# Performance work log

Measured on AMD Instinct MI355X. Metric: run time of the kernel, lower is better.

## Reference

```python
import jax, jax.numpy as jnp
import numpy as np

B, S, H, NH = 4, 2048, 768, 12
PH = H // NH  # per-head size


def setup_inputs() -> dict:
    key = jax.random.key(0)
    ks = jax.random.split(key, 12)
    s = 0.02
    return {
        "key": jax.random.normal(ks[0], (B, S, H), jnp.float32),
        "value": jax.random.normal(ks[1], (B, S, H), jnp.float32),
        "query": jax.random.normal(ks[2], (B, S, H), jnp.float32),
        "mask": jnp.zeros((B, 1, S, S), jnp.float32),  # additive mask
        "Wq": jax.random.normal(ks[3], (H, H), jnp.float32) * s,
        "bq": jnp.zeros((H,), jnp.float32),
        "Wk": jax.random.normal(ks[4], (H, H), jnp.float32) * s,
        "bk": jnp.zeros((H,), jnp.float32),
        "Wv": jax.random.normal(ks[5], (H, H), jnp.float32) * s,
        "bv": jnp.zeros((H,), jnp.float32),
        "Wo": jax.random.normal(ks[6], (H, H), jnp.float32) * s,
        "bo": jnp.zeros((H,), jnp.float32),
    }


def _heads(x):
    # [B,S,H] -> [B,NH,S,PH]
    return x.reshape(B, S, NH, PH).transpose(0, 2, 1, 3)


def reference(key, value, query, mask, Wq, bq, Wk, bk, Wv, bv, Wo, bo):
    # torch Linear: y = x @ W.T + b  (separate projections for q, k, v)
    q = _heads(query @ Wq.T + bq)
    k = _heads(key @ Wk.T + bk)
    v = _heads(value @ Wv.T + bv)
    scale = 1.0 / jnp.sqrt(jnp.asarray(PH, q.dtype))
    scores = jnp.einsum("bhqd,bhkd->bhqk", q, k) * scale + mask
    probs = jax.nn.softmax(scores, axis=-1)  # dropout p=0 -> identity
    out = jnp.einsum("bhqk,bhkd->bhqd", probs, v)
    out = out.transpose(0, 2, 1, 3).reshape(B, S, H)
    return out @ Wo.T + bo
```

## Files before the change

### kernel.cpp

```cpp
#include <hip/hip_runtime.h>
#include <hip/hip_bf16.h>
#include <cstddef>
#include <cstdint>

#define BB  4
#define SS  2048
#define HH  768
#define NHH 12
#define PHH 64
#define MM  (BB*SS)
#define LOG2E 1.4426950408889634f

typedef short         short8   __attribute__((ext_vector_type(8)));
typedef float         floatx4  __attribute__((ext_vector_type(4)));
typedef float         floatx16 __attribute__((ext_vector_type(16)));
typedef unsigned int  uint4v   __attribute__((ext_vector_type(4)));

static __device__ __forceinline__ unsigned short f2bf(float f) {
    unsigned int u = __float_as_uint(f);
    u += 0x7FFF + ((u >> 16) & 1);
    return (unsigned short)(u >> 16);
}

static __device__ __forceinline__ unsigned int cvtpk_bf16(float lo, float hi) {
    unsigned int r;
    asm("v_cvt_pk_bf16_f32 %0, %1, %2" : "=v"(r) : "v"(lo), "v"(hi));
    return r;
}

static __device__ __forceinline__ float v_exp2(float x) {
    float r;
    asm("v_exp_f32 %0, %1" : "=v"(r) : "v"(x));
    return r;
}

static __device__ __forceinline__ void plswap(unsigned int& a, unsigned int& b) {
    asm("v_permlane32_swap_b32 %0, %1" : "+v"(a), "+v"(b));
}

static __device__ __forceinline__ short8 mk_short8(unsigned int a, unsigned int b,
                                                   unsigned int c, unsigned int d) {
    uint4v u = {a, b, c, d};
    return __builtin_bit_cast(short8, u);
}

#define GLOAD_LDS16(g, l) __builtin_amdgcn_global_load_lds(            \
        (const __attribute__((address_space(1))) void*)(g),            \
        (__attribute__((address_space(3))) void*)(l), 16, 0, 0)

#define MFMA32(a, b, c) __builtin_amdgcn_mfma_f32_32x32x16_bf16((a), (b), (c), 0, 0, 0)

__global__ void mha_cvt_w4(const float* __restrict__ w0, const float* __restrict__ w1,
                           const float* __restrict__ w2, const float* __restrict__ w3,
                           unsigned short* __restrict__ dst,
                           unsigned int* __restrict__ fmask) {
    const int i = blockIdx.x * blockDim.x + threadIdx.x;
    if (blockIdx.x == 0 && threadIdx.x < 128) fmask[threadIdx.x] = 0u;
    const int which = i / 147456;
    const int j = i - which * 147456;
    const float* s = (which == 0) ? w0 : (which == 1) ? w1 : (which == 2) ? w2 : w3;
    float4 v = reinterpret_cast<const float4*>(s)[j];
    unsigned long long pk =
        (unsigned long long)f2bf(v.x)         |
        ((unsigned long long)f2bf(v.y) << 16) |
        ((unsigned long long)f2bf(v.z) << 32) |
        ((unsigned long long)f2bf(v.w) << 48);
    reinterpret_cast<unsigned long long*>(dst)[i] = pk;
}

__global__ void mha_mask_flags(const float* __restrict__ mask,
                               unsigned int* __restrict__ fmask) {
    int bid = blockIdx.x;
    int b   = bid >> 10;
    int rem = bid & 1023;
    int qt  = rem >> 5;
    int kt  = rem & 31;
    const float* base = mask + ((size_t)b*SS + (size_t)qt*64)*SS + kt*64;
    int t    = threadIdx.x;
    int lrow = t >> 4;
    int lcol = (t & 15) * 4;
    int nz = 0;
    #pragma unroll
    for (int i = 0; i < 4; ++i) {
        float4 v = *reinterpret_cast<const float4*>(base + (size_t)(lrow + 16*i)*SS + lcol);
        nz |= (v.x != 0.f) | (v.y != 0.f) | (v.z != 0.f) | (v.w != 0.f);
    }
    __shared__ int s;
    if (t == 0) s = 0;
    __syncthreads();
    if (nz) s = 1;
    __syncthreads();
    if (t == 0 && s) atomicOr(&fmask[b*32 + qt], 1u << kt);
}

template<int AIN_F32, int MODE>
__global__ __launch_bounds__(256) void mha_gemm(
        const void* __restrict__ Xv,
        const unsigned short* __restrict__ W,
        const float* __restrict__ bias,
        void* __restrict__ out) {
    __shared__ unsigned short As[64 * 32];
    __shared__ unsigned short Bs[128 * 32];
    const int wave = threadIdx.x >> 6;
    const int lane = threadIdx.x & 63;
    const int lq = lane & 15, lg = lane >> 4;
    const int m0 = blockIdx.x * 64;
    const int n0 = blockIdx.y * 128;
    const int srow = lane >> 2;
    const int scol = 8 * (lane & 3);

    const float* Xr32 = (const float*)Xv + (size_t)(m0 + wave*16 + srow)*HH + scol;
    const unsigned short* Xr16 = (const unsigned short*)Xv + (size_t)(m0 + wave*16 + srow)*HH + scol;
    const unsigned short* Wr0 = W + (size_t)(n0 + wave*32 + srow)*HH + scol;
    const unsigned short* Wr1 = W + (size_t)(n0 + wave*32 + 16 + srow)*HH + scol;
    unsigned short* As_d  = As + wave*512;
    unsigned short* As_w  = As + (wave*16 + srow)*32 + scol;
    unsigned short* Bs_d0 = Bs + wave*1024;
    unsigned short* Bs_d1 = Bs + wave*1024 + 512;

    floatx4 acc[4][2];
    #pragma unroll
    for (int m = 0; m < 4; ++m)
        #pragma unroll
        for (int n = 0; n < 2; ++n) acc[m][n] = (floatx4){0.f, 0.f, 0.f, 0.f};

    for (int k0 = 0; k0 < HH; k0 += 32) {
        if constexpr (AIN_F32) {
            float4 v0 = *reinterpret_cast<const float4*>(Xr32 + k0);
            float4 v1 = *reinterpret_cast<const float4*>(Xr32 + k0 + 4);
            GLOAD_LDS16(Wr0 + k0, Bs_d0);
            GLOAD_LDS16(Wr1 + k0, Bs_d1);
            uint4v u = { cvtpk_bf16(v0.x, v0.y), cvtpk_bf16(v0.z, v0.w),
                         cvtpk_bf16(v1.x, v1.y), cvtpk_bf16(v1.z, v1.w) };
            *reinterpret_cast<uint4v*>(As_w) = u;
        } else {
            GLOAD_LDS16(Xr16 + k0, As_d);
            GLOAD_LDS16(Wr0 + k0, Bs_d0);
            GLOAD_LDS16(Wr1 + k0, Bs_d1);
        }
        __syncthreads();
        short8 af[4], bw[2];
        #pragma unroll
        for (int m = 0; m < 4; ++m)
            af[m] = *reinterpret_cast<const short8*>(As + (16*m + lq)*32 + 8*lg);
        #pragma unroll
        for (int n = 0; n < 2; ++n)
            bw[n] = *reinterpret_cast<const short8*>(Bs + (32*wave + 16*n + lq)*32 + 8*lg);
        #pragma unroll
        for (int m = 0; m < 4; ++m)
            #pragma unroll
            for (int n = 0; n < 2; ++n)
                acc[m][n] = __builtin_amdgcn_mfma_f32_16x16x32_bf16(af[m], bw[n], acc[m][n], 0, 0, 0);
        __syncthreads();
    }

    #pragma unroll
    for (int n = 0; n < 2; ++n) {
        const int col = n0 + wave*32 + 16*n + lq;
        const float bv = bias[col];
        #pragma unroll
        for (int m = 0; m < 4; ++m) {
            #pragma unroll
            for (int r = 0; r < 4; ++r) {
                const int row = m0 + 16*m + 4*lg + r;
                float y = acc[m][n][r] + bv;
                if constexpr (MODE == 1) {
                    ((unsigned short*)out)[(size_t)row*HH + col] = f2bf(y * (0.125f * LOG2E));
                } else if constexpr (MODE == 3) {
                    ((float*)out)[(size_t)row*HH + col] = y;
                } else if constexpr (MODE == 4) {
                    int bb = row >> 11, s = row & 2047;
                    int hh = col >> 6,  d = col & 63;
                    int kt = s >> 6, half = (s >> 5) & 1, rr = s & 31;
                    int ks = d >> 4, h2 = (d >> 3) & 1, j = d & 7;
                    size_t idx = (((size_t)(bb*NHH + hh)*32 + kt)*4096)
                               + (half*4 + ks)*512 + (h2*32 + rr)*8 + j;
                    ((unsigned short*)out)[idx] = f2bf(y);
                } else {
                    int bb = row >> 11, s = row & 2047;
                    int hh = col >> 6,  d = col & 63;
                    int kt = s >> 6, ss = s & 63;
                    int ks = ss >> 4, h2 = (ss >> 3) & 1, j = ss & 7;
                    int vh = d >> 5, qq = d & 31;
                    size_t idx = (((size_t)(bb*NHH + hh)*32 + kt)*4096)
                               + (vh*4 + ks)*512 + (h2*32 + qq)*8 + j;
                    ((unsigned short*)out)[idx] = f2bf(y);
                }
            }
        }
    }
}

__global__ __launch_bounds__(256, 3) void mha_attn(
        const unsigned short* __restrict__ qb,
        const unsigned short* __restrict__ kfb,
        const unsigned short* __restrict__ vfb,
        const float* __restrict__ mask,
        const unsigned int* __restrict__ fmaskp,
        unsigned short* __restrict__ ab) {
    __shared__ unsigned short ldsbuf[2][8192];

    const int wave = threadIdx.x >> 6;
    const int lane = threadIdx.x & 63;
    const int ql   = lane & 31;
    const int hi   = lane >> 5;

    int bid = blockIdx.x;
    bid = (bid & 7) * 96 + (bid >> 3);
    const int qblk = bid & 15;
    int t = bid >> 4;
    const int h = t % NHH;
    const int b = t / NHH;

    const int q0 = qblk*128 + wave*32;
    const int q  = q0 + ql;

    const unsigned short* qp = qb + ((size_t)b*SS + q)*HH + h*PHH + 8*hi;
    short8 qf[4];
    #pragma unroll
    for (int ks = 0; ks < 4; ++ks)
        qf[ks] = *reinterpret_cast<const short8*>(qp + 16*ks);

    short8 ones;
    #pragma unroll
    for (int i = 0; i < 8; ++i) ones[i] = (short)0x3F80;

    const unsigned short* kvK = kfb + (size_t)(b*NHH + h) * 32 * 4096;
    const unsigned short* kvV = vfb + (size_t)(b*NHH + h) * 32 * 4096;
    const float* mrow = mask + ((size_t)b*SS + q)*SS;
    const unsigned int fm = fmaskp[b*32 + (q0 >> 6)];

    floatx16 o0, o1, lacc;
    #pragma unroll
    for (int i = 0; i < 16; ++i) { o0[i] = 0.f; o1[i] = 0.f; lacc[i] = 0.f; }

#define STAGE(bufi, kti)                                                       \
    {                                                                          \
        _Pragma("unroll")                                                      \
        for (int c = 0; c < 4; ++c) {                                          \
            const int ch = 4*wave + c;                                         \
            const unsigned short* src = (ch < 8)                               \
                ? (kvK + (size_t)(kti)*4096 + ch*512)                          \
                : (kvV + (size_t)(kti)*4096 + (ch - 8)*512);                   \
            GLOAD_LDS16(src + lane*8, &ldsbuf[bufi][ch*512]);                  \
        }                                                                      \
    }

    STAGE(0, 0)

    #pragma unroll 1
    for (int kt = 0; kt < 32; ++kt) {
        const int cur = kt & 1;
        STAGE(cur ^ 1, (kt + 1) & 31)

        asm volatile("s_waitcnt vmcnt(4)" ::: "memory");
        __builtin_amdgcn_sched_barrier(0);
        __builtin_amdgcn_s_barrier();

        const unsigned short* lk = &ldsbuf[cur][0];

        short8 kf[8];
        #pragma unroll
        for (int f = 0; f < 8; ++f)
            kf[f] = *reinterpret_cast<const short8*>(lk + f*512 + lane*8);
        floatx16 s0, s1;
        #pragma unroll
        for (int i = 0; i < 16; ++i) { s0[i] = 0.f; s1[i] = 0.f; }
        __builtin_amdgcn_s_setprio(1);
        #pragma unroll
        for (int ks = 0; ks < 4; ++ks) {
            s0 = MFMA32(kf[ks],   qf[ks], s0);
            s1 = MFMA32(kf[4+ks], qf[ks], s1);
        }
        __builtin_amdgcn_s_setprio(0);

        if (fm & (1u << kt)) {
            const float* mr = mrow + kt*64;
            #pragma unroll
            for (int g = 0; g < 4; ++g) {
                float4 a = *reinterpret_cast<const float4*>(mr + 8*g + 4*hi);
                float4 c = *reinterpret_cast<const float4*>(mr + 32 + 8*g + 4*hi);
                s0[4*g+0] = fmaf(a.x, LOG2E, s0[4*g+0]);
                s0[4*g+1] = fmaf(a.y, LOG2E, s0[4*g+1]);
                s0[4*g+2] = fmaf(a.z, LOG2E, s0[4*g+2]);
                s0[4*g+3] = fmaf(a.w, LOG2E, s0[4*g+3]);
                s1[4*g+0] = fmaf(c.x, LOG2E, s1[4*g+0]);
                s1[4*g+1] = fmaf(c.y, LOG2E, s1[4*g+1]);
                s1[4*g+2] = fmaf(c.z, LOG2E, s1[4*g+2]);
                s1[4*g+3] = fmaf(c.w, LOG2E, s1[4*g+3]);
            }
        }

        #pragma unroll
        for (int r = 0; r < 16; ++r) s0[r] = v_exp2(s0[r]);
        #pragma unroll
        for (int r = 0; r < 16; ++r) s1[r] = v_exp2(s1[r]);

        unsigned int c0 = cvtpk_bf16(s0[0],  s0[1]),  c1 = cvtpk_bf16(s0[2],  s0[3]);
        unsigned int c2 = cvtpk_bf16(s0[4],  s0[5]),  c3 = cvtpk_bf16(s0[6],  s0[7]);
        unsigned int c4 = cvtpk_bf16(s0[8],  s0[9]),  c5 = cvtpk_bf16(s0[10], s0[11]);
        unsigned int c6 = cvtpk_bf16(s0[12], s0[13]), c7 = cvtpk_bf16(s0[14], s0[15]);
        unsigned int d0 = cvtpk_bf16(s1[0],  s1[1]),  d1 = cvtpk_bf16(s1[2],  s1[3]);
        unsigned int d2 = cvtpk_bf16(s1[4],  s1[5]),  d3 = cvtpk_bf16(s1[6],  s1[7]);
        unsigned int d4 = cvtpk_bf16(s1[8],  s1[9]),  d5 = cvtpk_bf16(s1[10], s1[11]);
        unsigned int d6 = cvtpk_bf16(s1[12], s1[13]), d7 = cvtpk_bf16(s1[14], s1[15]);
        plswap(c0, c2); plswap(c1, c3); plswap(c4, c6); plswap(c5, c7);
        plswap(d0, d2); plswap(d1, d3); plswap(d4, d6); plswap(d5, d7);
        short8 pa[4];
        pa[0] = mk_short8(c0, c1, c2, c3);
        pa[1] = mk_short8(c4, c5, c6, c7);
        pa[2] = mk_short8(d0, d1, d2, d3);
        pa[3] = mk_short8(d4, d5, d6, d7);

        const unsigned short* lv = lk + 4096;
        short8 vf[8];
        #pragma unroll
        for (int g = 0; g < 8; ++g)
            vf[g] = *reinterpret_cast<const short8*>(lv + g*512 + lane*8);
        __builtin_amdgcn_s_setprio(1);
        #pragma unroll
        for (int ks = 0; ks < 4; ++ks) {
            o0   = MFMA32(vf[ks],   pa[ks], o0);
            o1   = MFMA32(vf[4+ks], pa[ks], o1);
            lacc = MFMA32(ones,     pa[ks], lacc);
        }
        __builtin_amdgcn_s_setprio(0);

        asm volatile("s_waitcnt lgkmcnt(0)" ::: "memory");
        __builtin_amdgcn_sched_barrier(0);
        __builtin_amdgcn_s_barrier();
    }
#undef STAGE

    const float inv = 1.f / lacc[0];
    unsigned short* op = ab + ((size_t)b*SS + q)*HH + h*PHH + 4*hi;
    #pragma unroll
    for (int g = 0; g < 4; ++g) {
        ushort4 w0, w1;
        w0.x = f2bf(o0[4*g+0]*inv); w0.y = f2bf(o0[4*g+1]*inv);
        w0.z = f2bf(o0[4*g+2]*inv); w0.w = f2bf(o0[4*g+3]*inv);
        w1.x = f2bf(o1[4*g+0]*inv); w1.y = f2bf(o1[4*g+1]*inv);
        w1.z = f2bf(o1[4*g+2]*inv); w1.w = f2bf(o1[4*g+3]*inv);
        *reinterpret_cast<ushort4*>(op + 8*g)      = w0;
        *reinterpret_cast<ushort4*>(op + 32 + 8*g) = w1;
    }
}

extern "C" void kernel_launch(void* const* d_in, const int* in_sizes, int n_in,
                              void* d_out, int out_size, void* d_ws, size_t ws_size,
                              hipStream_t stream) {
    const float* key   = (const float*)d_in[0];
    const float* value = (const float*)d_in[1];
    const float* query = (const float*)d_in[2];
    const float* mask  = (const float*)d_in[3];
    const float* Wq    = (const float*)d_in[4];
    const float* bq    = (const float*)d_in[5];
    const float* Wk    = (const float*)d_in[6];
    const float* bk    = (const float*)d_in[7];
    const float* Wv    = (const float*)d_in[8];
    const float* bv    = (const float*)d_in[9];
    const float* Wo    = (const float*)d_in[10];
    const float* bo    = (const float*)d_in[11];
    float* out = (float*)d_out;

    const size_t WSZ = (size_t)HH * HH;
    const size_t ASZ = (size_t)MM * HH;
    unsigned short* wqb = (unsigned short*)d_ws;
    unsigned short* wkb = wqb + WSZ;
    unsigned short* wvb = wkb + WSZ;
    unsigned short* wob = wvb + WSZ;
    unsigned short* qb  = wob + WSZ;
    unsigned short* kfb = qb + ASZ;
    unsigned short* vfb = kfb + ASZ;
    unsigned short* xb  = vfb + ASZ;
    unsigned int* fmask = (unsigned int*)(xb + ASZ);

    mha_cvt_w4<<<(4*147456)/256, 256, 0, stream>>>(Wq, Wk, Wv, Wo, wqb, fmask);

    mha_mask_flags<<<BB*32*32, 256, 0, stream>>>(mask, fmask);

    dim3 g(MM/64, HH/128);
    mha_gemm<1,1><<<g, 256, 0, stream>>>(query, wqb, bq, qb);
    mha_gemm<1,4><<<g, 256, 0, stream>>>(key,   wkb, bk, kfb);
    mha_gemm<1,5><<<g, 256, 0, stream>>>(value, wvb, bv, vfb);

    mha_attn<<<BB*NHH*(SS/128), 256, 0, stream>>>(qb, kfb, vfb, mask, fmask, xb);

    mha_gemm<0,3><<<g, 256, 0, stream>>>(xb, wob, bo, out);
}
```

Before: 172.4 us.

## Double-buffer projection GEMM with BK=64 and merge prep kernels

The projection GEMM now uses double-buffered LDS tiles with a K step of 64 instead of 32. Global loads for the next tile are issued before the MFMAs on the current tile, with explicit waitcnt and raw s_barrier replacing the two __syncthreads per step. The weight conversion and mask-flag kernels are merged into one launch. Mask flags become per-tile bytes instead of atomicOr bitmasks, and the attention kernel reassembles them into a bitmask. This costs more LDS, which may lower occupancy, and relies on hand-tuned vmcnt counts being correct.

```diff
diff --git a/kernel.cpp b/kernel.cpp
--- a/kernel.cpp
+++ b/kernel.cpp
@@ -50,47 +50,47 @@
 
 #define MFMA32(a, b, c) __builtin_amdgcn_mfma_f32_32x32x16_bf16((a), (b), (c), 0, 0, 0)
 
-__global__ void mha_cvt_w4(const float* __restrict__ w0, const float* __restrict__ w1,
-                           const float* __restrict__ w2, const float* __restrict__ w3,
-                           unsigned short* __restrict__ dst,
-                           unsigned int* __restrict__ fmask) {
-    const int i = blockIdx.x * blockDim.x + threadIdx.x;
-    if (blockIdx.x == 0 && threadIdx.x < 128) fmask[threadIdx.x] = 0u;
-    const int which = i / 147456;
-    const int j = i - which * 147456;
-    const float* s = (which == 0) ? w0 : (which == 1) ? w1 : (which == 2) ? w2 : w3;
-    float4 v = reinterpret_cast<const float4*>(s)[j];
-    unsigned long long pk =
-        (unsigned long long)f2bf(v.x)         |
-        ((unsigned long long)f2bf(v.y) << 16) |
-        ((unsigned long long)f2bf(v.z) << 32) |
-        ((unsigned long long)f2bf(v.w) << 48);
-    reinterpret_cast<unsigned long long*>(dst)[i] = pk;
-}
-
-__global__ void mha_mask_flags(const float* __restrict__ mask,
-                               unsigned int* __restrict__ fmask) {
-    int bid = blockIdx.x;
-    int b   = bid >> 10;
-    int rem = bid & 1023;
-    int qt  = rem >> 5;
-    int kt  = rem & 31;
-    const float* base = mask + ((size_t)b*SS + (size_t)qt*64)*SS + kt*64;
-    int t    = threadIdx.x;
-    int lrow = t >> 4;
-    int lcol = (t & 15) * 4;
-    int nz = 0;
-    #pragma unroll
-    for (int i = 0; i < 4; ++i) {
-        float4 v = *reinterpret_cast<const float4*>(base + (size_t)(lrow + 16*i)*SS + lcol);
-        nz |= (v.x != 0.f) | (v.y != 0.f) | (v.z != 0.f) | (v.w != 0.f);
-    }
-    __shared__ int s;
-    if (t == 0) s = 0;
-    __syncthreads();
-    if (nz) s = 1;
-    __syncthreads();
-    if (t == 0 && s) atomicOr(&fmask[b*32 + qt], 1u << kt);
+__global__ void mha_prep(const float* __restrict__ w0, const float* __restrict__ w1,
+                         const float* __restrict__ w2, const float* __restrict__ w3,
+                         unsigned short* __restrict__ dst,
+                         const float* __restrict__ mask,
+                         unsigned char* __restrict__ flags8) {
+    const int bid = blockIdx.x;
+    const int t = threadIdx.x;
+    if (bid < 2304) {
+        const int i = bid * 256 + t;
+        const int which = i / 147456;
+        const int j = i - which * 147456;
+        const float* s = (which == 0) ? w0 : (which == 1) ? w1 : (which == 2) ? w2 : w3;
+        float4 v = reinterpret_cast<const float4*>(s)[j];
+        unsigned long long pk =
+            (unsigned long long)f2bf(v.x)         |
+            ((unsigned long long)f2bf(v.y) << 16) |
+            ((unsigned long long)f2bf(v.z) << 32) |
+            ((unsigned long long)f2bf(v.w) << 48);
+        reinterpret_cast<unsigned long long*>(dst)[i] = pk;
+    } else {
+        const int fb = bid - 2304;
+        const int b  = fb >> 10;
+        const int rem = fb & 1023;
+        const int qt = rem >> 5;
+        const int kt = rem & 31;
+        const float* base = mask + ((size_t)b*SS + (size_t)qt*64)*SS + kt*64;
+        const int lrow = t >> 4;
+        const int lcol = (t & 15) * 4;
+        int nz = 0;
+        #pragma unroll
+        for (int i = 0; i < 4; ++i) {
+            float4 v = *reinterpret_cast<const float4*>(base + (size_t)(lrow + 16*i)*SS + lcol);
+            nz |= (v.x != 0.f) | (v.y != 0.f) | (v.z != 0.f) | (v.w != 0.f);
+        }
+        __shared__ int s;
+        if (t == 0) s = 0;
+        __syncthreads();
+        if (nz) s = 1;
+        __syncthreads();
+        if (t == 0) flags8[fb] = (unsigned char)s;
+    }
 }
 
 template<int AIN_F32, int MODE>
@@ -99,24 +99,39 @@
         const unsigned short* __restrict__ W,
         const float* __restrict__ bias,
         void* __restrict__ out) {
-    __shared__ unsigned short As[64 * 32];
-    __shared__ unsigned short Bs[128 * 32];
+    __shared__ unsigned short As[2][64 * 64];
+    __shared__ unsigned short Bs[2][128 * 64];
     const int wave = threadIdx.x >> 6;
     const int lane = threadIdx.x & 63;
     const int lq = lane & 15, lg = lane >> 4;
     const int m0 = blockIdx.x * 64;
     const int n0 = blockIdx.y * 128;
+    const int brow = lane >> 3;
+    const int bcol = 8 * (lane & 7);
     const int srow = lane >> 2;
-    const int scol = 8 * (lane & 3);
+    const int scol = 16 * (lane & 3);
 
     const float* Xr32 = (const float*)Xv + (size_t)(m0 + wave*16 + srow)*HH + scol;
-    const unsigned short* Xr16 = (const unsigned short*)Xv + (size_t)(m0 + wave*16 + srow)*HH + scol;
-    const unsigned short* Wr0 = W + (size_t)(n0 + wave*32 + srow)*HH + scol;
-    const unsigned short* Wr1 = W + (size_t)(n0 + wave*32 + 16 + srow)*HH + scol;
-    unsigned short* As_d  = As + wave*512;
-    unsigned short* As_w  = As + (wave*16 + srow)*32 + scol;
-    unsigned short* Bs_d0 = Bs + wave*1024;
-    unsigned short* Bs_d1 = Bs + wave*1024 + 512;
+
+#define STAGE_B(bi, k0)                                                        \
+    {                                                                          \
+        _Pragma("unroll")                                                      \
+        for (int c = 0; c < 4; ++c) {                                          \
+            const int ch = 4*wave + c;                                         \
+            GLOAD_LDS16(W + (size_t)(n0 + ch*8 + brow)*HH + (k0) + bcol,       \
+                        &Bs[bi][ch*512]);                                      \
+        }                                                                      \
+    }
+#define STAGE_A16(bi, k0)                                                      \
+    {                                                                          \
+        _Pragma("unroll")                                                      \
+        for (int c = 0; c < 2; ++c) {                                          \
+            const int ch = 2*wave + c;                                         \
+            GLOAD_LDS16((const unsigned short*)Xv                              \
+                            + (size_t)(m0 + ch*8 + brow)*HH + (k0) + bcol,     \
+                        &As[bi][ch*512]);                                      \
+        }                                                                      \
+    }
 
     floatx4 acc[4][2];
     #pragma unroll
@@ -124,35 +139,72 @@
         #pragma unroll
         for (int n = 0; n < 2; ++n) acc[m][n] = (floatx4){0.f, 0.f, 0.f, 0.f};
 
-    for (int k0 = 0; k0 < HH; k0 += 32) {
+    float4 a0, a1, a2, a3;
+    if constexpr (AIN_F32) {
+        a0 = *reinterpret_cast<const float4*>(Xr32);
+        a1 = *reinterpret_cast<const float4*>(Xr32 + 4);
+        a2 = *reinterpret_cast<const float4*>(Xr32 + 8);
+        a3 = *reinterpret_cast<const float4*>(Xr32 + 12);
+    } else {
+        STAGE_A16(0, 0)
+    }
+    STAGE_B(0, 0)
+
+    #pragma unroll 1
+    for (int t = 0; t < 12; ++t) {
+        const int cur = t & 1, nxt = cur ^ 1;
+        const int kN = ((t + 1) % 12) * 64;
+
         if constexpr (AIN_F32) {
-            float4 v0 = *reinterpret_cast<const float4*>(Xr32 + k0);
-            float4 v1 = *reinterpret_cast<const float4*>(Xr32 + k0 + 4);
-            GLOAD_LDS16(Wr0 + k0, Bs_d0);
-            GLOAD_LDS16(Wr1 + k0, Bs_d1);
-            uint4v u = { cvtpk_bf16(v0.x, v0.y), cvtpk_bf16(v0.z, v0.w),
-                         cvtpk_bf16(v1.x, v1.y), cvtpk_bf16(v1.z, v1.w) };
-            *reinterpret_cast<uint4v*>(As_w) = u;
+            unsigned short* aw = &As[cur][(wave*16 + srow)*64 + scol];
+            uint4v u0 = { cvtpk_bf16(a0.x, a0.y), cvtpk_bf16(a0.z, a0.w),
+                          cvtpk_bf16(a1.x, a1.y), cvtpk_bf16(a1.z, a1.w) };
+            uint4v u1 = { cvtpk_bf16(a2.x, a2.y), cvtpk_bf16(a2.z, a2.w),
+                          cvtpk_bf16(a3.x, a3.y), cvtpk_bf16(a3.z, a3.w) };
+            *reinterpret_cast<uint4v*>(aw) = u0;
+            *reinterpret_cast<uint4v*>(aw + 8) = u1;
+            a0 = *reinterpret_cast<const float4*>(Xr32 + kN);
+            a1 = *reinterpret_cast<const float4*>(Xr32 + kN + 4);
+            a2 = *reinterpret_cast<const float4*>(Xr32 + kN + 8);
+            a3 = *reinterpret_cast<const float4*>(Xr32 + kN + 12);
+            STAGE_B(nxt, kN)
+            asm volatile("s_waitcnt vmcnt(8) lgkmcnt(0)" ::: "memory");
         } else {
-            GLOAD_LDS16(Xr16 + k0, As_d);
-            GLOAD_LDS16(Wr0 + k0, Bs_d0);
-            GLOAD_LDS16(Wr1 + k0, Bs_d1);
-        }
-        __syncthreads();
-        short8 af[4], bw[2];
-        #pragma unroll
-        for (int m = 0; m < 4; ++m)
-            af[m] = *reinterpret_cast<const short8*>(As + (16*m + lq)*32 + 8*lg);
-        #pragma unroll
-        for (int n = 0; n < 2; ++n)
-            bw[n] = *reinterpret_cast<const short8*>(Bs + (32*wave + 16*n + lq)*32 + 8*lg);
+            STAGE_A16(nxt, kN)
+            STAGE_B(nxt, kN)
+            asm volatile("s_waitcnt vmcnt(6)" ::: "memory");
+        }
+        __builtin_amdgcn_sched_barrier(0);
+        __builtin_amdgcn_s_barrier();
+
+        short8 af[4][2], bw[2][2];
         #pragma unroll
         for (int m = 0; m < 4; ++m)
             #pragma unroll
-            for (int n = 0; n < 2; ++n)
-                acc[m][n] = __builtin_amdgcn_mfma_f32_16x16x32_bf16(af[m], bw[n], acc[m][n], 0, 0, 0);
-        __syncthreads();
-    }
+            for (int kk = 0; kk < 2; ++kk)
+                af[m][kk] = *reinterpret_cast<const short8*>(
+                                &As[cur][(16*m + lq)*64 + 32*kk + 8*lg]);
+        #pragma unroll
+        for (int n = 0; n < 2; ++n)
+            #pragma unroll
+            for (int kk = 0; kk < 2; ++kk)
+                bw[n][kk] = *reinterpret_cast<const short8*>(
+                                &Bs[cur][(32*wave + 16*n + lq)*64 + 32*kk + 8*lg]);
+        #pragma unroll
+        for (int kk = 0; kk < 2; ++kk)
+            #pragma unroll
+            for (int m = 0; m < 4; ++m)
+                #pragma unroll
+                for (int n = 0; n < 2; ++n)
+                    acc[m][n] = __builtin_amdgcn_mfma_f32_16x16x32_bf16(
+                                    af[m][kk], bw[n][kk], acc[m][n], 0, 0, 0);
+
+        asm volatile("s_waitcnt lgkmcnt(0)" ::: "memory");
+        __builtin_amdgcn_sched_barrier(0);
+        __builtin_amdgcn_s_barrier();
+    }
+#undef STAGE_B
+#undef STAGE_A16
 
     #pragma unroll
     for (int n = 0; n < 2; ++n) {
@@ -196,7 +248,7 @@
         const unsigned short* __restrict__ kfb,
         const unsigned short* __restrict__ vfb,
         const float* __restrict__ mask,
-        const unsigned int* __restrict__ fmaskp,
+        const unsigned char* __restrict__ flags8,
         unsigned short* __restrict__ ab) {
     __shared__ unsigned short ldsbuf[2][8192];
 
@@ -228,7 +280,17 @@
     const unsigned short* kvK = kfb + (size_t)(b*NHH + h) * 32 * 4096;
     const unsigned short* kvV = vfb + (size_t)(b*NHH + h) * 32 * 4096;
     const float* mrow = mask + ((size_t)b*SS + q)*SS;
-    const unsigned int fm = fmaskp[b*32 + (q0 >> 6)];
+
+    unsigned int fm = 0;
+    {
+        const unsigned int* fw = (const unsigned int*)(flags8 + b*1024 + (q0 >> 6)*32);
+        #pragma unroll
+        for (int i = 0; i < 8; ++i) {
+            unsigned int w = fw[i];
+            fm |= ((w & 1u) << (4*i))       | (((w >> 8) & 1u) << (4*i + 1))
+                | (((w >> 16) & 1u) << (4*i + 2)) | (((w >> 24) & 1u) << (4*i + 3));
+        }
+    }
 
     floatx16 o0, o1, lacc;
     #pragma unroll
@@ -373,18 +435,16 @@
     unsigned short* kfb = qb + ASZ;
     unsigned short* vfb = kfb + ASZ;
     unsigned short* xb  = vfb + ASZ;
-    unsigned int* fmask = (unsigned int*)(xb + ASZ);
-
-    mha_cvt_w4<<<(4*147456)/256, 256, 0, stream>>>(Wq, Wk, Wv, Wo, wqb, fmask);
-
-    mha_mask_flags<<<BB*32*32, 256, 0, stream>>>(mask, fmask);
+    unsigned char* flags8 = (unsigned char*)(xb + ASZ);
+
+    mha_prep<<<2304 + 4096, 256, 0, stream>>>(Wq, Wk, Wv, Wo, wqb, mask, flags8);
 
     dim3 g(MM/64, HH/128);
     mha_gemm<1,1><<<g, 256, 0, stream>>>(query, wqb, bq, qb);
     mha_gemm<1,4><<<g, 256, 0, stream>>>(key,   wkb, bk, kfb);
     mha_gemm<1,5><<<g, 256, 0, stream>>>(value, wvb, bv, vfb);
 
-    mha_attn<<<BB*NHH*(SS/128), 256, 0, stream>>>(qb, kfb, vfb, mask, fmask, xb);
+    mha_attn<<<BB*NHH*(SS/128), 256, 0, stream>>>(qb, kfb, vfb, mask, flags8, xb);
 
     mha_gemm<0,3><<<g, 256, 0, stream>>>(xb, wob, bo, out);
 }
```

Measured after the change: 174.7 us. No clear change (+1.4%).
